# Kernel optimization log

Measured on AMD Instinct MI355X. Metric: run time of the kernel, lower is better.

Reference implementation:

```python
import jax, jax.numpy as jnp
import numpy as np

EPS = 0.25  # diffusion-map epsilon

def setup_inputs() -> dict:
    key = jax.random.key(0)
    ks = jax.random.split(key, 6)
    B, N, F, L = 8, 2048, 256, 16
    s = lambda fan_in: 1.0 / np.sqrt(fan_in)
    return {
        "x":      jax.random.normal(ks[0], (B, N, F), dtype=jnp.float32),
        "proj_w": jax.random.normal(ks[1], (L, F), dtype=jnp.float32) * s(F),
        "proj_b": jnp.zeros((L,), dtype=jnp.float32),
        "pi_w1":  jax.random.normal(ks[2], (F, L), dtype=jnp.float32) * s(L),
        "pi_b1":  jnp.zeros((F,), dtype=jnp.float32),
        "pi_w2":  jax.random.normal(ks[3], (1, F), dtype=jnp.float32) * s(F),
        "pi_b2":  jnp.zeros((1,), dtype=jnp.float32),
        "dt":     jnp.array([0.1], dtype=jnp.float32),
    }

def reference(x, proj_w, proj_b, pi_w1, pi_b1, pi_w2, pi_b2, dt):
    # z = proj(x): [B, N, L]
    z = jnp.einsum("bnf,lf->bnl", x, proj_w) + proj_b
    # pairwise squared distances via expansion (avoids [B,N,N,L] intermediate)
    sq = jnp.sum(z * z, axis=-1)                              # [B, N]
    gram = jnp.einsum("bnl,bml->bnm", z, z)                   # [B, N, N]
    d2 = jnp.maximum(sq[:, :, None] + sq[:, None, :] - 2.0 * gram, 0.0)
    K = jnp.exp(-d2 / (4.0 * EPS))                            # K_epsilon [B,N,N]
    q = jnp.sum(K, axis=2)                                    # q_epsilon_tilde [B,N]
    # pi(z): MLP 16 -> 256 -> 1 with ReLU then Sigmoid
    h = jax.nn.relu(jnp.einsum("bnl,fl->bnf", z, pi_w1) + pi_b1)
    pi_v = jax.nn.sigmoid(jnp.einsum("bnf,of->bno", h, pi_w2) + pi_b2)[..., 0]  # [B,N]
    # K_tilde = K @ diag(pi/q): scale columns
    Kt = K * (pi_v / q)[:, None, :]                            # [B,N,N]
    row = jnp.sum(Kt, axis=2) + 1e-5                           # diag of D_tilde
    # L = (1/eps) * D_tilde^{-1} K_tilde - I ; inverse of diagonal = reciprocal
    # L @ x computed without materializing identity:
    Lx = (1.0 / EPS) * jnp.einsum("bnm,bmf->bnf", Kt / row[:, :, None], x) - x
    return x + dt[0] * Lx
```

## Files before the change

### kernel.cpp

```cpp
#include <hip/hip_runtime.h>
#include <hip/hip_bf16.h>

#define BATCH 8
#define NN    2048
#define FF    256
#define LL    16

typedef float f32x4 __attribute__((ext_vector_type(4)));
typedef short s16x8 __attribute__((ext_vector_type(8)));

static __device__ __forceinline__ unsigned short f2bf(float f) {
    return __builtin_bit_cast(unsigned short, __float2bfloat16(f));
}
static __device__ __forceinline__ float bf2f(unsigned short u) {
    unsigned int x = ((unsigned int)u) << 16;
    return __builtin_bit_cast(float, x);
}

typedef const __attribute__((address_space(1))) unsigned int glb_uint;
typedef __attribute__((address_space(3))) unsigned int lds_uint;
static __device__ __forceinline__ void gload_lds16(const void* g, void* l) {
    __builtin_amdgcn_global_load_lds((glb_uint*)g, (lds_uint*)l, 16, 0, 0);
}

__global__ __launch_bounds__(256) void fused_a_kernel(
    const float* __restrict__ x,
    const float* __restrict__ proj_w, const float* __restrict__ proj_b,
    const float* __restrict__ pi_w1,  const float* __restrict__ pi_b1,
    const float* __restrict__ pi_w2,  const float* __restrict__ pi_b2,
    unsigned short* __restrict__ xT,
    unsigned short* __restrict__ zbG,
    float* __restrict__ sqbuf,
    float* __restrict__ pibuf)
{
    const int bid = blockIdx.x;
    const int b = bid & 7, nt = bid >> 3;
    const int n0 = nt * 32;
    const int t = threadIdx.x;
    const int wv = t >> 6, ln = t & 63;
    const int kg = ln >> 4, cl = ln & 15;

    const float* xb = x + (size_t)b * NN * FF;
    unsigned short* xTb = xT + (size_t)b * FF * NN;

    __shared__ unsigned short xbsh[32 * 268];
    __shared__ unsigned short Wbsh[16 * 268];
    __shared__ unsigned short W1bsh[256 * 24];
    __shared__ unsigned short zbsh[32 * 24];
    __shared__ float b1sh[256], w2sh[256], pbsh[16];
    __shared__ float pp[2][32];

#pragma unroll
    for (int i = 0; i < 8; ++i) {
        const int slot = i * 256 + t;
        const int r = slot >> 6, c4 = slot & 63;
        const float4 v = *(const float4*)(xb + (size_t)(n0 + r) * FF + c4 * 4);
        ushort4 o; o.x = f2bf(v.x); o.y = f2bf(v.y); o.z = f2bf(v.z); o.w = f2bf(v.w);
        *(ushort4*)&xbsh[r * 268 + c4 * 4] = o;
    }
#pragma unroll
    for (int i = 0; i < 4; ++i) {
        const int slot = i * 256 + t;
        const int l = slot >> 6, c4 = slot & 63;
        const float4 v = *(const float4*)(proj_w + l * FF + c4 * 4);
        ushort4 o; o.x = f2bf(v.x); o.y = f2bf(v.y); o.z = f2bf(v.z); o.w = f2bf(v.w);
        *(ushort4*)&Wbsh[l * 268 + c4 * 4] = o;
    }
#pragma unroll
    for (int i = 0; i < 4; ++i) {
        const int slot = i * 256 + t;
        const int f = slot >> 2, q = slot & 3;
        const float4 v = *(const float4*)(pi_w1 + f * LL + q * 4);
        ushort4 o; o.x = f2bf(v.x); o.y = f2bf(v.y); o.z = f2bf(v.z); o.w = f2bf(v.w);
        *(ushort4*)&W1bsh[f * 24 + q * 4] = o;
    }
    b1sh[t] = pi_b1[t];
    w2sh[t] = pi_w2[t];
    if (t < 16) pbsh[t] = proj_b[t];
    __syncthreads();

    if (wv < 2) {
        f32x4 zacc = {0.f, 0.f, 0.f, 0.f};
#pragma unroll
        for (int g = 0; g < 8; ++g) {
            const s16x8 af = *(const s16x8*)&xbsh[(wv * 16 + cl) * 268 + g * 32 + kg * 8];
            const s16x8 bf = *(const s16x8*)&Wbsh[cl * 268 + g * 32 + kg * 8];
            zacc = __builtin_amdgcn_mfma_f32_16x16x32_bf16(af, bf, zacc, 0, 0, 0);
        }
        const float pb = pbsh[cl];
#pragma unroll
        for (int r = 0; r < 4; ++r)
            zbsh[(wv * 16 + kg * 4 + r) * 24 + cl] = f2bf(zacc[r] + pb);
    } else {
#pragma unroll
        for (int it = 0; it < 16; ++it) {
            const int f = (wv - 2) * 128 + it * 8 + (ln >> 3);
            const int q = ln & 7;
            ushort4 o;
            o.x = xbsh[(q * 4 + 0) * 268 + f];
            o.y = xbsh[(q * 4 + 1) * 268 + f];
            o.z = xbsh[(q * 4 + 2) * 268 + f];
            o.w = xbsh[(q * 4 + 3) * 268 + f];
            *(ushort4*)(xTb + (size_t)f * NN + n0 + q * 4) = o;
        }
    }
    __syncthreads();

    if (t < 32) {
        unsigned short zr[16]; float sq = 0.f;
#pragma unroll
        for (int l = 0; l < 16; ++l) {
            zr[l] = zbsh[t * 24 + l];
            const float zf = bf2f(zr[l]);
            sq = fmaf(zf, zf, sq);
        }
        unsigned short* dst = zbG + ((size_t)b * NN + n0 + t) * 16;
        *(uint4*)dst = *(uint4*)&zr[0];
        *(uint4*)(dst + 8) = *(uint4*)&zr[8];
        sqbuf[(size_t)b * NN + n0 + t] = sq;
    }

    {
        const int ntl = wv & 1;
        s16x8 bz = {0, 0, 0, 0, 0, 0, 0, 0};
        if (kg < 2) bz = *(const s16x8*)&zbsh[(ntl * 16 + cl) * 24 + kg * 8];
        float pisum = 0.f;
        const f32x4 zf4 = {0.f, 0.f, 0.f, 0.f};
#pragma unroll
        for (int j = 0; j < 8; ++j) {
            const int ft = (wv >> 1) * 8 + j;
            s16x8 aw = {0, 0, 0, 0, 0, 0, 0, 0};
            if (kg < 2) aw = *(const s16x8*)&W1bsh[(ft * 16 + cl) * 24 + kg * 8];
            const f32x4 h4 = __builtin_amdgcn_mfma_f32_16x16x32_bf16(aw, bz, zf4, 0, 0, 0);
#pragma unroll
            for (int r = 0; r < 4; ++r) {
                const int f = ft * 16 + kg * 4 + r;
                const float h = fmaxf(h4[r] + b1sh[f], 0.f);
                pisum = fmaf(h, w2sh[f], pisum);
            }
        }
        pisum += __shfl_xor(pisum, 16, 64);
        pisum += __shfl_xor(pisum, 32, 64);
        if (ln < 16) pp[wv >> 1][ntl * 16 + ln] = pisum;
    }
    __syncthreads();

    if (t < 32) {
        const float tp = pp[0][t] + pp[1][t] + pi_b2[0];
        pibuf[(size_t)b * NN + n0 + t] = 1.f / (1.f + __expf(-tp));
    }
}

__global__ __launch_bounds__(256) void qc_kernel(
    const unsigned short* __restrict__ zbG,
    const float* __restrict__ sqbuf,
    const float* __restrict__ pibuf,
    float* __restrict__ cbuf)
{
    const int bid = blockIdx.x;
    const int b = bid & 7, nt = bid >> 3;
    const int n0 = nt * 32;
    const int t = threadIdx.x;
    const int wv = t >> 6, ln = t & 63;
    const int kg = ln >> 4, cl = ln & 15;

    const unsigned short* zb = zbG + (size_t)b * NN * LL;
    const float* sqb = sqbuf + (size_t)b * NN;

    __shared__ unsigned short zsh[2][256 * 24];
    __shared__ float sqh[2][256];
    __shared__ float qq[2][32];

    s16x8 zn = {0, 0, 0, 0, 0, 0, 0, 0};
    if (kg < 2) zn = *(const s16x8*)(zb + (size_t)(n0 + (wv & 1) * 16 + cl) * 16 + kg * 8);
    const float sqn = sqb[n0 + (wv & 1) * 16 + cl];
    const f32x4 zf4 = {0.f, 0.f, 0.f, 0.f};
    float qloc = 0.f;

    uint4 za = *(const uint4*)(zb + (size_t)t * 16);
    uint4 zc = *(const uint4*)(zb + (size_t)t * 16 + 8);
    float sv = sqb[t];
    *(uint4*)&zsh[0][t * 24] = za;
    *(uint4*)&zsh[0][t * 24 + 8] = zc;
    sqh[0][t] = sv;
    __syncthreads();

    const int mbase = (wv >> 1) * 128;
    for (int ch = 0; ch < 8; ++ch) {
        const int cur = ch & 1;
        if (ch < 7) {
            const int m = (ch + 1) * 256 + t;
            za = *(const uint4*)(zb + (size_t)m * 16);
            zc = *(const uint4*)(zb + (size_t)m * 16 + 8);
            sv = sqb[m];
        }
#pragma unroll
        for (int mt = 0; mt < 8; ++mt) {
            s16x8 zm = {0, 0, 0, 0, 0, 0, 0, 0};
            if (kg < 2) zm = *(const s16x8*)&zsh[cur][(mbase + mt * 16 + cl) * 24 + kg * 8];
            const f32x4 g = __builtin_amdgcn_mfma_f32_16x16x32_bf16(zm, zn, zf4, 0, 0, 0);
            const f32x4 sq4 = *(const f32x4*)&sqh[cur][mbase + mt * 16 + kg * 4];
#pragma unroll
            for (int r = 0; r < 4; ++r)
                qloc += __expf(2.f * g[r] - sq4[r] - sqn);
        }
        if (ch < 7) {
            *(uint4*)&zsh[cur ^ 1][t * 24] = za;
            *(uint4*)&zsh[cur ^ 1][t * 24 + 8] = zc;
            sqh[cur ^ 1][t] = sv;
        }
        __syncthreads();
    }
    qloc += __shfl_xor(qloc, 16, 64);
    qloc += __shfl_xor(qloc, 32, 64);
    if (ln < 16) qq[wv >> 1][(wv & 1) * 16 + ln] = qloc;
    __syncthreads();
    if (t < 32) {
        const size_t gi = (size_t)b * NN + n0 + t;
        cbuf[gi] = pibuf[gi] / (qq[0][t] + qq[1][t]);
    }
}

struct ZM { s16x8 z[4]; };

__global__ __launch_bounds__(256) void main_kernel(
    const float* __restrict__ x,
    const unsigned short* __restrict__ xT,
    const unsigned short* __restrict__ zbG,
    const float* __restrict__ sqbuf,
    const float* __restrict__ cbuf,
    const float* __restrict__ dtp,
    float* __restrict__ out)
{
    const int bid = blockIdx.x;
    const int b = bid & 7;
    const int rest = bid >> 3;
    const int fs = rest & 1;
    const int nt = rest >> 1;
    const int n0 = nt * 64, f0 = fs * 128;
    const int t = threadIdx.x;
    const int wv = t >> 6, ln = t & 63;
    const int kg = ln >> 4, cl = ln & 15;

    const float*          xb  = x   + (size_t)b * NN * FF;
    const unsigned short* xTb = xT  + (size_t)b * FF * NN;
    const unsigned short* zb  = zbG + (size_t)b * NN * LL;
    const float*          sqB = sqbuf + (size_t)b * NN;
    const float*          cB  = cbuf  + (size_t)b * NN;
    float*                ob  = out + (size_t)b * NN * FF;

    __shared__ unsigned short xsh[2][128 * 64];
    __shared__ unsigned short wsh[2][64 * 64];
    __shared__ float csh[2][64], sqsh[2][64];
    __shared__ float rsp[64];

    const float dtv = dtp[0];
    const int nloc = wv * 16 + cl;

    s16x8 zn = {0, 0, 0, 0, 0, 0, 0, 0};
    if (kg < 2) zn = *(const s16x8*)(zb + (size_t)(n0 + nloc) * 16 + kg * 8);
    const float sqn = sqB[n0 + nloc];
    const f32x4 zf4 = {0.f, 0.f, 0.f, 0.f};

    f32x4 acc[2][4];
#pragma unroll
    for (int fi = 0; fi < 2; ++fi)
#pragma unroll
        for (int ni = 0; ni < 4; ++ni) acc[fi][ni] = (f32x4){0.f, 0.f, 0.f, 0.f};
    float rloc = 0.f;

    auto loadZM = [&](ZM& Z, int kt) {
        const int m0 = kt * 64;
#pragma unroll
        for (int mt = 0; mt < 4; ++mt) {
            Z.z[mt] = (s16x8){0, 0, 0, 0, 0, 0, 0, 0};
            if (kg < 2)
                Z.z[mt] = *(const s16x8*)(zb + (size_t)(m0 + mt * 16 + cl) * 16 + kg * 8);
        }
    };
    auto STAGE_CS = [&](int buf, int kt) {
        const int m0 = kt * 64;
        if (t < 64)        csh[buf][t]       = cB[m0 + t];
        else if (t < 128)  sqsh[buf][t - 64] = sqB[m0 + t - 64];
    };
    auto ISSUE = [&](int buf, int kt) {
        const int m0 = kt * 64;
        char* dst = (char*)&xsh[buf][0];
#pragma unroll
        for (int i = 0; i < 4; ++i) {
            const int fl = (i * 4 + wv) * 8 + (ln >> 3);
            const int cp = ln & 7;
            const int clog = cp ^ (fl & 7);
            const unsigned short* src = xTb + (size_t)(f0 + fl) * NN + m0 + clog * 8;
            gload_lds16(src, dst + (i * 4 + wv) * 1024);
        }
    };
    auto P1 = [&](const ZM& Z, int cur) {
        char* wb = (char*)&wsh[cur][0];
#pragma unroll
        for (int mt = 0; mt < 4; ++mt) {
            const f32x4 g = __builtin_amdgcn_mfma_f32_16x16x32_bf16(Z.z[mt], zn, zf4, 0, 0, 0);
            const f32x4 sq4 = *(const f32x4*)&sqsh[cur][mt * 16 + kg * 4];
            const f32x4 cm4 = *(const f32x4*)&csh[cur][mt * 16 + kg * 4];
            const float w0 = __expf(2.f * g[0] - sq4[0] - sqn) * cm4[0];
            const float w1 = __expf(2.f * g[1] - sq4[1] - sqn) * cm4[1];
            const float w2 = __expf(2.f * g[2] - sq4[2] - sqn) * cm4[2];
            const float w3 = __expf(2.f * g[3] - sq4[3] - sqn) * cm4[3];
            rloc += (w0 + w1) + (w2 + w3);
            uint2 val;
            val.x = (unsigned)f2bf(w0) | ((unsigned)f2bf(w1) << 16);
            val.y = (unsigned)f2bf(w2) | ((unsigned)f2bf(w3) << 16);
            const int c16 = mt * 2 + (kg >> 1);
            const int phys = c16 ^ (nloc & 7);
            *(uint2*)(wb + nloc * 128 + phys * 16 + (kg & 1) * 8) = val;
        }
    };
    auto P2 = [&](int cur) {
        const char* xbuf = (const char*)&xsh[cur][0];
        const char* wbuf = (const char*)&wsh[cur][0];
#pragma unroll
        for (int ks = 0; ks < 2; ++ks) {
            s16x8 a[2], bw[4];
#pragma unroll
            for (int fi = 0; fi < 2; ++fi) {
                const int fl = wv * 32 + fi * 16 + cl;
                const int slot = (ks * 4 + kg) ^ (fl & 7);
                a[fi] = *(const s16x8*)(xbuf + fl * 128 + slot * 16);
            }
#pragma unroll
            for (int ni = 0; ni < 4; ++ni) {
                const int nr = ni * 16 + cl;
                const int slot = (ks * 4 + kg) ^ (nr & 7);
                bw[ni] = *(const s16x8*)(wbuf + nr * 128 + slot * 16);
            }
#pragma unroll
            for (int fi = 0; fi < 2; ++fi)
#pragma unroll
                for (int ni = 0; ni < 4; ++ni)
                    acc[fi][ni] = __builtin_amdgcn_mfma_f32_16x16x32_bf16(
                        a[fi], bw[ni], acc[fi][ni], 0, 0, 0);
        }
    };

    ZM zA, zB;
    STAGE_CS(0, 0);
    loadZM(zA, 0);
    ISSUE(0, 0);
    __syncthreads();

    for (int kt = 0; kt < 32; kt += 2) {
        P1(zA, 0);
        { loadZM(zB, kt + 1); STAGE_CS(1, kt + 1); }
        __syncthreads();
        ISSUE(1, kt + 1);
        __builtin_amdgcn_s_setprio(1);
        P2(0);
        __builtin_amdgcn_s_setprio(0);
        P1(zB, 1);
        if (kt + 2 < 32) { loadZM(zA, kt + 2); STAGE_CS(0, kt + 2); }
        __syncthreads();
        if (kt + 2 < 32) ISSUE(0, kt + 2);
        __builtin_amdgcn_s_setprio(1);
        P2(1);
        __builtin_amdgcn_s_setprio(0);
    }

    rloc += __shfl_xor(rloc, 16, 64);
    rloc += __shfl_xor(rloc, 32, 64);
    if (ln < 16) rsp[wv * 16 + ln] = rloc;
    __syncthreads();

#pragma unroll
    for (int ni = 0; ni < 4; ++ni) {
        const int nl = ni * 16 + cl;
        const float sc = 4.f * dtv / (rsp[nl] + 1e-5f);
        const int ng = n0 + nl;
#pragma unroll
        for (int fi = 0; fi < 2; ++fi) {
            const int fg = f0 + wv * 32 + fi * 16 + kg * 4;
            const float4 xv = *(const float4*)(xb + (size_t)ng * FF + fg);
            float4 o;
            o.x = (1.f - dtv) * xv.x + sc * acc[fi][ni][0];
            o.y = (1.f - dtv) * xv.y + sc * acc[fi][ni][1];
            o.z = (1.f - dtv) * xv.z + sc * acc[fi][ni][2];
            o.w = (1.f - dtv) * xv.w + sc * acc[fi][ni][3];
            *(float4*)(ob + (size_t)ng * FF + fg) = o;
        }
    }
}

extern "C" void kernel_launch(void* const* d_in, const int* in_sizes, int n_in,
                              void* d_out, int out_size, void* d_ws, size_t ws_size,
                              hipStream_t stream) {
    const float* x      = (const float*)d_in[0];
    const float* proj_w = (const float*)d_in[1];
    const float* proj_b = (const float*)d_in[2];
    const float* pi_w1  = (const float*)d_in[3];
    const float* pi_b1  = (const float*)d_in[4];
    const float* pi_w2  = (const float*)d_in[5];
    const float* pi_b2  = (const float*)d_in[6];
    const float* dtp    = (const float*)d_in[7];
    float* out = (float*)d_out;

    unsigned short* xT  = (unsigned short*)d_ws;
    unsigned short* zbG = xT + (size_t)BATCH * FF * NN;
    float* sqbuf = (float*)(zbG + (size_t)BATCH * NN * LL);
    float* pibuf = sqbuf + (size_t)BATCH * NN;
    float* cbuf  = pibuf + (size_t)BATCH * NN;

    fused_a_kernel<<<dim3(BATCH * (NN / 32)), dim3(256), 0, stream>>>(
        x, proj_w, proj_b, pi_w1, pi_b1, pi_w2, pi_b2, xT, zbG, sqbuf, pibuf);

    qc_kernel<<<dim3(BATCH * (NN / 32)), dim3(256), 0, stream>>>(
        zbG, sqbuf, pibuf, cbuf);

    main_kernel<<<dim3(BATCH * (NN / 64) * 2), dim3(256), 0, stream>>>(
        x, xT, zbG, sqbuf, cbuf, dtp, out);
}
```

Before: 148.3 us.

## Fuse three kernels into one persistent kernel with grid barriers and 32x32 MFMA

```diff
diff --git a/kernel.cpp b/kernel.cpp
--- a/kernel.cpp
+++ b/kernel.cpp
@@ -5,9 +5,12 @@
 #define NN    2048
 #define FF    256
 #define LL    16
-
-typedef float f32x4 __attribute__((ext_vector_type(4)));
-typedef short s16x8 __attribute__((ext_vector_type(8)));
+#define GRID  512
+
+typedef float f32x4  __attribute__((ext_vector_type(4)));
+typedef float f32x16 __attribute__((ext_vector_type(16)));
+typedef short s16x8  __attribute__((ext_vector_type(8)));
+typedef unsigned int u32;
 
 static __device__ __forceinline__ unsigned short f2bf(float f) {
     return __builtin_bit_cast(unsigned short, __float2bfloat16(f));
@@ -23,368 +26,344 @@
     __builtin_amdgcn_global_load_lds((glb_uint*)g, (lds_uint*)l, 16, 0, 0);
 }
 
-__global__ __launch_bounds__(256) void fused_a_kernel(
+union Smem {
+    struct {
+        unsigned short xbsh[32 * 268];
+        unsigned short Wbsh[16 * 268];
+        unsigned short W1bsh[256 * 24];
+        unsigned short zbsh[32 * 24];
+        float b1sh[256], w2sh[256], pbsh[16];
+        float pp[2][32];
+    } a;
+    struct {
+        unsigned short zsh[2][256 * 24];
+        float sqh[2][256];
+        float qq[2][32];
+    } q;
+    struct {
+        unsigned short xsh[2][8192];
+        float rsp[4][32];
+    } m;
+};
+
+static __device__ __forceinline__ void gsync(unsigned* cnt) {
+    __syncthreads();
+    if (threadIdx.x == 0) {
+        __threadfence();
+        __hip_atomic_fetch_add(cnt, 1u, __ATOMIC_ACQ_REL, __HIP_MEMORY_SCOPE_AGENT);
+        while (__hip_atomic_load(cnt, __ATOMIC_ACQUIRE, __HIP_MEMORY_SCOPE_AGENT) < GRID) {
+            __builtin_amdgcn_s_sleep(2);
+        }
+    }
+    __syncthreads();
+    __threadfence();
+}
+
+__global__ __launch_bounds__(256, 2) void tmd_fused(
     const float* __restrict__ x,
     const float* __restrict__ proj_w, const float* __restrict__ proj_b,
     const float* __restrict__ pi_w1,  const float* __restrict__ pi_b1,
     const float* __restrict__ pi_w2,  const float* __restrict__ pi_b2,
+    const float* __restrict__ dtp,
     unsigned short* __restrict__ xT,
     unsigned short* __restrict__ zbG,
     float* __restrict__ sqbuf,
-    float* __restrict__ pibuf)
+    float* __restrict__ pibuf,
+    float* __restrict__ cebuf,
+    unsigned* __restrict__ syncA,
+    unsigned* __restrict__ syncQ,
+    float* __restrict__ out)
 {
+    __shared__ Smem sm;
     const int bid = blockIdx.x;
-    const int b = bid & 7, nt = bid >> 3;
-    const int n0 = nt * 32;
+    const int b = bid & 7;
     const int t = threadIdx.x;
     const int wv = t >> 6, ln = t & 63;
     const int kg = ln >> 4, cl = ln & 15;
 
     const float* xb = x + (size_t)b * NN * FF;
     unsigned short* xTb = xT + (size_t)b * FF * NN;
-
-    __shared__ unsigned short xbsh[32 * 268];
-    __shared__ unsigned short Wbsh[16 * 268];
-    __shared__ unsigned short W1bsh[256 * 24];
-    __shared__ unsigned short zbsh[32 * 24];
-    __shared__ float b1sh[256], w2sh[256], pbsh[16];
-    __shared__ float pp[2][32];
-
-#pragma unroll
-    for (int i = 0; i < 8; ++i) {
-        const int slot = i * 256 + t;
-        const int r = slot >> 6, c4 = slot & 63;
-        const float4 v = *(const float4*)(xb + (size_t)(n0 + r) * FF + c4 * 4);
-        ushort4 o; o.x = f2bf(v.x); o.y = f2bf(v.y); o.z = f2bf(v.z); o.w = f2bf(v.w);
-        *(ushort4*)&xbsh[r * 268 + c4 * 4] = o;
+    unsigned short* zbW = zbG + (size_t)b * NN * LL;
+    const unsigned short* zb = zbG + (size_t)b * NN * LL;
+    float* sqW = sqbuf + (size_t)b * NN;
+    const float* sqB = sqbuf + (size_t)b * NN;
+
+    {
+        const int nt = bid >> 3;
+        const int n0 = nt * 32;
+        auto& A = sm.a;
+
+#pragma unroll
+        for (int i = 0; i < 8; ++i) {
+            const int slot = i * 256 + t;
+            const int r = slot >> 6, c4 = slot & 63;
+            const float4 v = *(const float4*)(xb + (size_t)(n0 + r) * FF + c4 * 4);
+            ushort4 o; o.x = f2bf(v.x); o.y = f2bf(v.y); o.z = f2bf(v.z); o.w = f2bf(v.w);
+            *(ushort4*)&A.xbsh[r * 268 + c4 * 4] = o;
+        }
+#pragma unroll
+        for (int i = 0; i < 4; ++i) {
+            const int slot = i * 256 + t;
+            const int l = slot >> 6, c4 = slot & 63;
+            const float4 v = *(const float4*)(proj_w + l * FF + c4 * 4);
+            ushort4 o; o.x = f2bf(v.x); o.y = f2bf(v.y); o.z = f2bf(v.z); o.w = f2bf(v.w);
+            *(ushort4*)&A.Wbsh[l * 268 + c4 * 4] = o;
+        }
+#pragma unroll
+        for (int i = 0; i < 4; ++i) {
+            const int slot = i * 256 + t;
+            const int f = slot >> 2, q = slot & 3;
+            const float4 v = *(const float4*)(pi_w1 + f * LL + q * 4);
+            ushort4 o; o.x = f2bf(v.x); o.y = f2bf(v.y); o.z = f2bf(v.z); o.w = f2bf(v.w);
+            *(ushort4*)&A.W1bsh[f * 24 + q * 4] = o;
+        }
+        A.b1sh[t] = pi_b1[t];
+        A.w2sh[t] = pi_w2[t];
+        if (t < 16) A.pbsh[t] = proj_b[t];
+        __syncthreads();
+
+        if (wv < 2) {
+            f32x4 zacc = {0.f, 0.f, 0.f, 0.f};
+#pragma unroll
+            for (int g = 0; g < 8; ++g) {
+                const s16x8 af = *(const s16x8*)&A.xbsh[(wv * 16 + cl) * 268 + g * 32 + kg * 8];
+                const s16x8 bf = *(const s16x8*)&A.Wbsh[cl * 268 + g * 32 + kg * 8];
+                zacc = __builtin_amdgcn_mfma_f32_16x16x32_bf16(af, bf, zacc, 0, 0, 0);
+            }
+            const float pb = A.pbsh[cl];
+#pragma unroll
+            for (int r = 0; r < 4; ++r)
+                A.zbsh[(wv * 16 + kg * 4 + r) * 24 + cl] = f2bf(zacc[r] + pb);
+        } else {
+#pragma unroll
+            for (int it = 0; it < 16; ++it) {
+                const int f = (wv - 2) * 128 + it * 8 + (ln >> 3);
+                const int q = ln & 7;
+                ushort4 o;
+                o.x = A.xbsh[(q * 4 + 0) * 268 + f];
+                o.y = A.xbsh[(q * 4 + 1) * 268 + f];
+                o.z = A.xbsh[(q * 4 + 2) * 268 + f];
+                o.w = A.xbsh[(q * 4 + 3) * 268 + f];
+                *(ushort4*)(xTb + (size_t)f * NN + n0 + q * 4) = o;
+            }
+        }
+        __syncthreads();
+
+        if (t < 32) {
+            unsigned short zr[16]; float sq = 0.f;
+#pragma unroll
+            for (int l = 0; l < 16; ++l) {
+                zr[l] = A.zbsh[t * 24 + l];
+                const float zf = bf2f(zr[l]);
+                sq = fmaf(zf, zf, sq);
+            }
+            unsigned short* dst = zbW + (size_t)(n0 + t) * 16;
+            *(uint4*)dst = *(uint4*)&zr[0];
+            *(uint4*)(dst + 8) = *(uint4*)&zr[8];
+            sqW[n0 + t] = sq;
+        }
+
+        {
+            const int ntl = wv & 1;
+            s16x8 bz = {0, 0, 0, 0, 0, 0, 0, 0};
+            if (kg < 2) bz = *(const s16x8*)&A.zbsh[(ntl * 16 + cl) * 24 + kg * 8];
+            float pisum = 0.f;
+            const f32x4 zf4 = {0.f, 0.f, 0.f, 0.f};
+#pragma unroll
+            for (int j = 0; j < 8; ++j) {
+                const int ft = (wv >> 1) * 8 + j;
+                s16x8 aw = {0, 0, 0, 0, 0, 0, 0, 0};
+                if (kg < 2) aw = *(const s16x8*)&A.W1bsh[(ft * 16 + cl) * 24 + kg * 8];
+                const f32x4 h4 = __builtin_amdgcn_mfma_f32_16x16x32_bf16(aw, bz, zf4, 0, 0, 0);
+#pragma unroll
+                for (int r = 0; r < 4; ++r) {
+                    const int f = ft * 16 + kg * 4 + r;
+                    const float hh = fmaxf(h4[r] + A.b1sh[f], 0.f);
+                    pisum = fmaf(hh, A.w2sh[f], pisum);
+                }
+            }
+            pisum += __shfl_xor(pisum, 16, 64);
+            pisum += __shfl_xor(pisum, 32, 64);
+            if (ln < 16) A.pp[wv >> 1][ntl * 16 + ln] = pisum;
+        }
+        __syncthreads();
+        if (t < 32) {
+            const float tp = A.pp[0][t] + A.pp[1][t] + pi_b2[0];
+            pibuf[(size_t)b * NN + n0 + t] = 1.f / (1.f + __expf(-tp));
+        }
     }
-#pragma unroll
-    for (int i = 0; i < 4; ++i) {
-        const int slot = i * 256 + t;
-        const int l = slot >> 6, c4 = slot & 63;
-        const float4 v = *(const float4*)(proj_w + l * FF + c4 * 4);
-        ushort4 o; o.x = f2bf(v.x); o.y = f2bf(v.y); o.z = f2bf(v.z); o.w = f2bf(v.w);
-        *(ushort4*)&Wbsh[l * 268 + c4 * 4] = o;
+
+    gsync(syncA);
+
+    {
+        const int nt = bid >> 3;
+        const int n0 = nt * 32;
+        auto& Q = sm.q;
+
+        s16x8 zn = {0, 0, 0, 0, 0, 0, 0, 0};
+        if (kg < 2) zn = *(const s16x8*)(zb + (size_t)(n0 + (wv & 1) * 16 + cl) * 16 + kg * 8);
+        const float sqn = sqB[n0 + (wv & 1) * 16 + cl];
+        const f32x4 zf4 = {0.f, 0.f, 0.f, 0.f};
+        float qloc = 0.f;
+
+        uint4 za = *(const uint4*)(zb + (size_t)t * 16);
+        uint4 zc = *(const uint4*)(zb + (size_t)t * 16 + 8);
+        float sv = sqB[t];
+        *(uint4*)&Q.zsh[0][t * 24] = za;
+        *(uint4*)&Q.zsh[0][t * 24 + 8] = zc;
+        Q.sqh[0][t] = sv;
+        __syncthreads();
+
+        const int mbase = (wv >> 1) * 128;
+        for (int ch = 0; ch < 8; ++ch) {
+            const int cur = ch & 1;
+            if (ch < 7) {
+                const int m = (ch + 1) * 256 + t;
+                za = *(const uint4*)(zb + (size_t)m * 16);
+                zc = *(const uint4*)(zb + (size_t)m * 16 + 8);
+                sv = sqB[m];
+            }
+#pragma unroll
+            for (int mt = 0; mt < 8; ++mt) {
+                s16x8 zm = {0, 0, 0, 0, 0, 0, 0, 0};
+                if (kg < 2) zm = *(const s16x8*)&Q.zsh[cur][(mbase + mt * 16 + cl) * 24 + kg * 8];
+                const f32x4 g = __builtin_amdgcn_mfma_f32_16x16x32_bf16(zm, zn, zf4, 0, 0, 0);
+                const f32x4 sq4 = *(const f32x4*)&Q.sqh[cur][mbase + mt * 16 + kg * 4];
+#pragma unroll
+                for (int r = 0; r < 4; ++r)
+                    qloc += __expf(2.f * g[r] - sq4[r] - sqn);
+            }
+            if (ch < 7) {
+                *(uint4*)&Q.zsh[cur ^ 1][t * 24] = za;
+                *(uint4*)&Q.zsh[cur ^ 1][t * 24 + 8] = zc;
+                Q.sqh[cur ^ 1][t] = sv;
+            }
+            __syncthreads();
+        }
+        qloc += __shfl_xor(qloc, 16, 64);
+        qloc += __shfl_xor(qloc, 32, 64);
+        if (ln < 16) Q.qq[wv >> 1][(wv & 1) * 16 + ln] = qloc;
+        __syncthreads();
+        if (t < 32) {
+            const size_t gi = (size_t)b * NN + n0 + t;
+            cebuf[gi] = pibuf[gi] / (Q.qq[0][t] + Q.qq[1][t]) * __expf(-sqB[n0 + t]);
+        }
     }
-#pragma unroll
-    for (int i = 0; i < 4; ++i) {
-        const int slot = i * 256 + t;
-        const int f = slot >> 2, q = slot & 3;
-        const float4 v = *(const float4*)(pi_w1 + f * LL + q * 4);
-        ushort4 o; o.x = f2bf(v.x); o.y = f2bf(v.y); o.z = f2bf(v.z); o.w = f2bf(v.w);
-        *(ushort4*)&W1bsh[f * 24 + q * 4] = o;
-    }
-    b1sh[t] = pi_b1[t];
-    w2sh[t] = pi_w2[t];
-    if (t < 16) pbsh[t] = proj_b[t];
-    __syncthreads();
-
-    if (wv < 2) {
-        f32x4 zacc = {0.f, 0.f, 0.f, 0.f};
-#pragma unroll
-        for (int g = 0; g < 8; ++g) {
-            const s16x8 af = *(const s16x8*)&xbsh[(wv * 16 + cl) * 268 + g * 32 + kg * 8];
-            const s16x8 bf = *(const s16x8*)&Wbsh[cl * 268 + g * 32 + kg * 8];
-            zacc = __builtin_amdgcn_mfma_f32_16x16x32_bf16(af, bf, zacc, 0, 0, 0);
-        }
-        const float pb = pbsh[cl];
-#pragma unroll
-        for (int r = 0; r < 4; ++r)
-            zbsh[(wv * 16 + kg * 4 + r) * 24 + cl] = f2bf(zacc[r] + pb);
-    } else {
-#pragma unroll
-        for (int it = 0; it < 16; ++it) {
-            const int f = (wv - 2) * 128 + it * 8 + (ln >> 3);
-            const int q = ln & 7;
-            ushort4 o;
-            o.x = xbsh[(q * 4 + 0) * 268 + f];
-            o.y = xbsh[(q * 4 + 1) * 268 + f];
-            o.z = xbsh[(q * 4 + 2) * 268 + f];
-            o.w = xbsh[(q * 4 + 3) * 268 + f];
-            *(ushort4*)(xTb + (size_t)f * NN + n0 + q * 4) = o;
-        }
-    }
-    __syncthreads();
-
-    if (t < 32) {
-        unsigned short zr[16]; float sq = 0.f;
-#pragma unroll
-        for (int l = 0; l < 16; ++l) {
-            zr[l] = zbsh[t * 24 + l];
-            const float zf = bf2f(zr[l]);
-            sq = fmaf(zf, zf, sq);
-        }
-        unsigned short* dst = zbG + ((size_t)b * NN + n0 + t) * 16;
-        *(uint4*)dst = *(uint4*)&zr[0];
-        *(uint4*)(dst + 8) = *(uint4*)&zr[8];
-        sqbuf[(size_t)b * NN + n0 + t] = sq;
-    }
+
+    gsync(syncQ);
 
     {
-        const int ntl = wv & 1;
-        s16x8 bz = {0, 0, 0, 0, 0, 0, 0, 0};
-        if (kg < 2) bz = *(const s16x8*)&zbsh[(ntl * 16 + cl) * 24 + kg * 8];
-        float pisum = 0.f;
-        const f32x4 zf4 = {0.f, 0.f, 0.f, 0.f};
-#pragma unroll
-        for (int j = 0; j < 8; ++j) {
-            const int ft = (wv >> 1) * 8 + j;
-            s16x8 aw = {0, 0, 0, 0, 0, 0, 0, 0};
-            if (kg < 2) aw = *(const s16x8*)&W1bsh[(ft * 16 + cl) * 24 + kg * 8];
-            const f32x4 h4 = __builtin_amdgcn_mfma_f32_16x16x32_bf16(aw, bz, zf4, 0, 0, 0);
-#pragma unroll
-            for (int r = 0; r < 4; ++r) {
-                const int f = ft * 16 + kg * 4 + r;
-                const float h = fmaxf(h4[r] + b1sh[f], 0.f);
-                pisum = fmaf(h, w2sh[f], pisum);
-            }
-        }
-        pisum += __shfl_xor(pisum, 16, 64);
-        pisum += __shfl_xor(pisum, 32, 64);
-        if (ln < 16) pp[wv >> 1][ntl * 16 + ln] = pisum;
-    }
-    __syncthreads();
-
-    if (t < 32) {
-        const float tp = pp[0][t] + pp[1][t] + pi_b2[0];
-        pibuf[(size_t)b * NN + n0 + t] = 1.f / (1.f + __expf(-tp));
-    }
-}
-
-__global__ __launch_bounds__(256) void qc_kernel(
-    const unsigned short* __restrict__ zbG,
-    const float* __restrict__ sqbuf,
-    const float* __restrict__ pibuf,
-    float* __restrict__ cbuf)
-{
-    const int bid = blockIdx.x;
-    const int b = bid & 7, nt = bid >> 3;
-    const int n0 = nt * 32;
-    const int t = threadIdx.x;
-    const int wv = t >> 6, ln = t & 63;
-    const int kg = ln >> 4, cl = ln & 15;
-
-    const unsigned short* zb = zbG + (size_t)b * NN * LL;
-    const float* sqb = sqbuf + (size_t)b * NN;
-
-    __shared__ unsigned short zsh[2][256 * 24];
-    __shared__ float sqh[2][256];
-    __shared__ float qq[2][32];
-
-    s16x8 zn = {0, 0, 0, 0, 0, 0, 0, 0};
-    if (kg < 2) zn = *(const s16x8*)(zb + (size_t)(n0 + (wv & 1) * 16 + cl) * 16 + kg * 8);
-    const float sqn = sqb[n0 + (wv & 1) * 16 + cl];
-    const f32x4 zf4 = {0.f, 0.f, 0.f, 0.f};
-    float qloc = 0.f;
-
-    uint4 za = *(const uint4*)(zb + (size_t)t * 16);
-    uint4 zc = *(const uint4*)(zb + (size_t)t * 16 + 8);
-    float sv = sqb[t];
-    *(uint4*)&zsh[0][t * 24] = za;
-    *(uint4*)&zsh[0][t * 24 + 8] = zc;
-    sqh[0][t] = sv;
-    __syncthreads();
-
-    const int mbase = (wv >> 1) * 128;
-    for (int ch = 0; ch < 8; ++ch) {
-        const int cur = ch & 1;
-        if (ch < 7) {
-            const int m = (ch + 1) * 256 + t;
-            za = *(const uint4*)(zb + (size_t)m * 16);
-            zc = *(const uint4*)(zb + (size_t)m * 16 + 8);
-            sv = sqb[m];
-        }
-#pragma unroll
-        for (int mt = 0; mt < 8; ++mt) {
-            s16x8 zm = {0, 0, 0, 0, 0, 0, 0, 0};
-            if (kg < 2) zm = *(const s16x8*)&zsh[cur][(mbase + mt * 16 + cl) * 24 + kg * 8];
-            const f32x4 g = __builtin_amdgcn_mfma_f32_16x16x32_bf16(zm, zn, zf4, 0, 0, 0);
-            const f32x4 sq4 = *(const f32x4*)&sqh[cur][mbase + mt * 16 + kg * 4];
-#pragma unroll
-            for (int r = 0; r < 4; ++r)
-                qloc += __expf(2.f * g[r] - sq4[r] - sqn);
-        }
-        if (ch < 7) {
-            *(uint4*)&zsh[cur ^ 1][t * 24] = za;
-            *(uint4*)&zsh[cur ^ 1][t * 24 + 8] = zc;
-            sqh[cur ^ 1][t] = sv;
-        }
-        __syncthreads();
-    }
-    qloc += __shfl_xor(qloc, 16, 64);
-    qloc += __shfl_xor(qloc, 32, 64);
-    if (ln < 16) qq[wv >> 1][(wv & 1) * 16 + ln] = qloc;
-    __syncthreads();
-    if (t < 32) {
-        const size_t gi = (size_t)b * NN + n0 + t;
-        cbuf[gi] = pibuf[gi] / (qq[0][t] + qq[1][t]);
-    }
-}
-
-struct ZM { s16x8 z[4]; };
-
-__global__ __launch_bounds__(256) void main_kernel(
-    const float* __restrict__ x,
-    const unsigned short* __restrict__ xT,
-    const unsigned short* __restrict__ zbG,
-    const float* __restrict__ sqbuf,
-    const float* __restrict__ cbuf,
-    const float* __restrict__ dtp,
-    float* __restrict__ out)
-{
-    const int bid = blockIdx.x;
-    const int b = bid & 7;
-    const int rest = bid >> 3;
-    const int fs = rest & 1;
-    const int nt = rest >> 1;
-    const int n0 = nt * 64, f0 = fs * 128;
-    const int t = threadIdx.x;
-    const int wv = t >> 6, ln = t & 63;
-    const int kg = ln >> 4, cl = ln & 15;
-
-    const float*          xb  = x   + (size_t)b * NN * FF;
-    const unsigned short* xTb = xT  + (size_t)b * FF * NN;
-    const unsigned short* zb  = zbG + (size_t)b * NN * LL;
-    const float*          sqB = sqbuf + (size_t)b * NN;
-    const float*          cB  = cbuf  + (size_t)b * NN;
-    float*                ob  = out + (size_t)b * NN * FF;
-
-    __shared__ unsigned short xsh[2][128 * 64];
-    __shared__ unsigned short wsh[2][64 * 64];
-    __shared__ float csh[2][64], sqsh[2][64];
-    __shared__ float rsp[64];
-
-    const float dtv = dtp[0];
-    const int nloc = wv * 16 + cl;
-
-    s16x8 zn = {0, 0, 0, 0, 0, 0, 0, 0};
-    if (kg < 2) zn = *(const s16x8*)(zb + (size_t)(n0 + nloc) * 16 + kg * 8);
-    const float sqn = sqB[n0 + nloc];
-    const f32x4 zf4 = {0.f, 0.f, 0.f, 0.f};
-
-    f32x4 acc[2][4];
-#pragma unroll
-    for (int fi = 0; fi < 2; ++fi)
-#pragma unroll
-        for (int ni = 0; ni < 4; ++ni) acc[fi][ni] = (f32x4){0.f, 0.f, 0.f, 0.f};
-    float rloc = 0.f;
-
-    auto loadZM = [&](ZM& Z, int kt) {
-        const int m0 = kt * 64;
-#pragma unroll
-        for (int mt = 0; mt < 4; ++mt) {
-            Z.z[mt] = (s16x8){0, 0, 0, 0, 0, 0, 0, 0};
-            if (kg < 2)
-                Z.z[mt] = *(const s16x8*)(zb + (size_t)(m0 + mt * 16 + cl) * 16 + kg * 8);
-        }
-    };
-    auto STAGE_CS = [&](int buf, int kt) {
-        const int m0 = kt * 64;
-        if (t < 64)        csh[buf][t]       = cB[m0 + t];
-        else if (t < 128)  sqsh[buf][t - 64] = sqB[m0 + t - 64];
-    };
-    auto ISSUE = [&](int buf, int kt) {
-        const int m0 = kt * 64;
-        char* dst = (char*)&xsh[buf][0];
-#pragma unroll
-        for (int i = 0; i < 4; ++i) {
-            const int fl = (i * 4 + wv) * 8 + (ln >> 3);
-            const int cp = ln & 7;
-            const int clog = cp ^ (fl & 7);
-            const unsigned short* src = xTb + (size_t)(f0 + fl) * NN + m0 + clog * 8;
-            gload_lds16(src, dst + (i * 4 + wv) * 1024);
-        }
-    };
-    auto P1 = [&](const ZM& Z, int cur) {
-        char* wb = (char*)&wsh[cur][0];
-#pragma unroll
-        for (int mt = 0; mt < 4; ++mt) {
-            const f32x4 g = __builtin_amdgcn_mfma_f32_16x16x32_bf16(Z.z[mt], zn, zf4, 0, 0, 0);
-            const f32x4 sq4 = *(const f32x4*)&sqsh[cur][mt * 16 + kg * 4];
-            const f32x4 cm4 = *(const f32x4*)&csh[cur][mt * 16 + kg * 4];
-            const float w0 = __expf(2.f * g[0] - sq4[0] - sqn) * cm4[0];
-            const float w1 = __expf(2.f * g[1] - sq4[1] - sqn) * cm4[1];
-            const float w2 = __expf(2.f * g[2] - sq4[2] - sqn) * cm4[2];
-            const float w3 = __expf(2.f * g[3] - sq4[3] - sqn) * cm4[3];
-            rloc += (w0 + w1) + (w2 + w3);
-            uint2 val;
-            val.x = (unsigned)f2bf(w0) | ((unsigned)f2bf(w1) << 16);
-            val.y = (unsigned)f2bf(w2) | ((unsigned)f2bf(w3) << 16);
-            const int c16 = mt * 2 + (kg >> 1);
-            const int phys = c16 ^ (nloc & 7);
-            *(uint2*)(wb + nloc * 128 + phys * 16 + (kg & 1) * 8) = val;
-        }
-    };
-    auto P2 = [&](int cur) {
-        const char* xbuf = (const char*)&xsh[cur][0];
-        const char* wbuf = (const char*)&wsh[cur][0];
-#pragma unroll
-        for (int ks = 0; ks < 2; ++ks) {
-            s16x8 a[2], bw[4];
-#pragma unroll
-            for (int fi = 0; fi < 2; ++fi) {
-                const int fl = wv * 32 + fi * 16 + cl;
-                const int slot = (ks * 4 + kg) ^ (fl & 7);
-                a[fi] = *(const s16x8*)(xbuf + fl * 128 + slot * 16);
-            }
-#pragma unroll
-            for (int ni = 0; ni < 4; ++ni) {
-                const int nr = ni * 16 + cl;
-                const int slot = (ks * 4 + kg) ^ (nr & 7);
-                bw[ni] = *(const s16x8*)(wbuf + nr * 128 + slot * 16);
-            }
-#pragma unroll
-            for (int fi = 0; fi < 2; ++fi)
-#pragma unroll
-                for (int ni = 0; ni < 4; ++ni)
-                    acc[fi][ni] = __builtin_amdgcn_mfma_f32_16x16x32_bf16(
-                        a[fi], bw[ni], acc[fi][ni], 0, 0, 0);
-        }
-    };
-
-    ZM zA, zB;
-    STAGE_CS(0, 0);
-    loadZM(zA, 0);
-    ISSUE(0, 0);
-    __syncthreads();
-
-    for (int kt = 0; kt < 32; kt += 2) {
-        P1(zA, 0);
-        { loadZM(zB, kt + 1); STAGE_CS(1, kt + 1); }
-        __syncthreads();
-        ISSUE(1, kt + 1);
-        __builtin_amdgcn_s_setprio(1);
-        P2(0);
-        __builtin_amdgcn_s_setprio(0);
-        P1(zB, 1);
-        if (kt + 2 < 32) { loadZM(zA, kt + 2); STAGE_CS(0, kt + 2); }
-        __syncthreads();
-        if (kt + 2 < 32) ISSUE(0, kt + 2);
-        __builtin_amdgcn_s_setprio(1);
-        P2(1);
-        __builtin_amdgcn_s_setprio(0);
-    }
-
-    rloc += __shfl_xor(rloc, 16, 64);
-    rloc += __shfl_xor(rloc, 32, 64);
-    if (ln < 16) rsp[wv * 16 + ln] = rloc;
-    __syncthreads();
-
-#pragma unroll
-    for (int ni = 0; ni < 4; ++ni) {
-        const int nl = ni * 16 + cl;
-        const float sc = 4.f * dtv / (rsp[nl] + 1e-5f);
-        const int ng = n0 + nl;
-#pragma unroll
-        for (int fi = 0; fi < 2; ++fi) {
-            const int fg = f0 + wv * 32 + fi * 16 + kg * 4;
-            const float4 xv = *(const float4*)(xb + (size_t)ng * FF + fg);
-            float4 o;
-            o.x = (1.f - dtv) * xv.x + sc * acc[fi][ni][0];
-            o.y = (1.f - dtv) * xv.y + sc * acc[fi][ni][1];
-            o.z = (1.f - dtv) * xv.z + sc * acc[fi][ni][2];
-            o.w = (1.f - dtv) * xv.w + sc * acc[fi][ni][3];
-            *(float4*)(ob + (size_t)ng * FF + fg) = o;
+        const int fs = (bid >> 3) & 1;
+        const int nt = bid >> 4;
+        const int n0 = nt * 64, f0 = fs * 128;
+        const int i31 = ln & 31, h = ln >> 5;
+        const int nt_w = wv & 1, fs_w = wv >> 1;
+
+        const float* ceB = cebuf + (size_t)b * NN;
+        float* ob = out + (size_t)b * NN * FF;
+        const float dtv = dtp[0];
+
+        const f32x16 Z16 = {0.f,0.f,0.f,0.f,0.f,0.f,0.f,0.f,
+                            0.f,0.f,0.f,0.f,0.f,0.f,0.f,0.f};
+
+        const s16x8 zn = *(const s16x8*)(zb + (size_t)(n0 + nt_w * 32 + i31) * 16 + h * 8);
+        const float sqn = sqB[n0 + nt_w * 32 + i31];
+
+        f32x16 acc0 = Z16, acc1 = Z16;
+        float rloc = 0.f;
+
+        auto ISSUE = [&](char* dstBase, int kt) {
+            const int m0 = kt * 64;
+#pragma unroll
+            for (int i = 0; i < 4; ++i) {
+                const int fl = (i * 4 + wv) * 8 + (ln >> 3);
+                const int cp = ln & 7;
+                const int clog = cp ^ (fl & 7);
+                gload_lds16(xTb + (size_t)(f0 + fl) * NN + m0 + clog * 8,
+                            dstBase + (i * 4 + wv) * 1024);
+            }
+        };
+        auto LOADZM = [&](int mG) -> s16x8 {
+            return *(const s16x8*)(zb + (size_t)(mG + i31) * 16 + h * 8);
+        };
+
+        auto COMPUTE = [&](int kt, const char* xbuf,
+                           const s16x8 zc0, const s16x8 zc1,
+                           s16x8& zn0, s16x8& zn1, int ktN) {
+            s16x8 Afr[2][2];
+#pragma unroll
+            for (int g = 0; g < 2; ++g) {
+                const s16x8 zm = g ? zc1 : zc0;
+                const int mG = kt * 64 + g * 32;
+                const f32x16 gD = __builtin_amdgcn_mfma_f32_32x32x16_bf16(zm, zn, Z16, 0, 0, 0);
+                u32 pk[8];
+#pragma unroll
+                for (int q = 0; q < 4; ++q) {
+                    const f32x4 ce4 = *(const f32x4*)(ceB + mG + 4 * h + 8 * q);
+                    const float w0 = __expf(2.f * gD[q * 4 + 0] - sqn) * ce4[0];
+                    const float w1 = __expf(2.f * gD[q * 4 + 1] - sqn) * ce4[1];
+                    const float w2 = __expf(2.f * gD[q * 4 + 2] - sqn) * ce4[2];
+                    const float w3 = __expf(2.f * gD[q * 4 + 3] - sqn) * ce4[3];
+                    rloc += (w0 + w1) + (w2 + w3);
+                    pk[q * 2 + 0] = (u32)f2bf(w0) | ((u32)f2bf(w1) << 16);
+                    pk[q * 2 + 1] = (u32)f2bf(w2) | ((u32)f2bf(w3) << 16);
+                }
+                u32 sw[8];
+#pragma unroll
+                for (int p = 0; p < 8; ++p) sw[p] = (u32)__shfl_xor((int)pk[p], 32, 64);
+                union { u32 u[4]; s16x8 v; } a0, a1;
+                a0.u[0] = h ? sw[2] : pk[0];  a0.u[1] = h ? sw[3] : pk[1];
+                a0.u[2] = h ? pk[2] : sw[0];  a0.u[3] = h ? pk[3] : sw[1];
+                a1.u[0] = h ? sw[6] : pk[4];  a1.u[1] = h ? sw[7] : pk[5];
+                a1.u[2] = h ? pk[6] : sw[4];  a1.u[3] = h ? pk[7] : sw[5];
+                Afr[g][0] = a0.v;  Afr[g][1] = a1.v;
+            }
+            zn0 = LOADZM(ktN * 64);
+            zn1 = LOADZM(ktN * 64 + 32);
+            const int fl0 = fs_w * 64 + i31;
+            const int fl1 = fl0 + 32;
+#pragma unroll
+            for (int g = 0; g < 2; ++g)
+#pragma unroll
+                for (int mk = 0; mk < 2; ++mk) {
+                    const int c = g * 4 + mk * 2 + h;
+                    const s16x8 B0 = *(const s16x8*)(xbuf + fl0 * 128 + (c ^ (fl0 & 7)) * 16);
+                    acc0 = __builtin_amdgcn_mfma_f32_32x32x16_bf16(Afr[g][mk], B0, acc0, 0, 0, 0);
+                    const s16x8 B1 = *(const s16x8*)(xbuf + fl1 * 128 + (c ^ (fl1 & 7)) * 16);
+                    acc1 = __builtin_amdgcn_mfma_f32_32x32x16_bf16(Afr[g][mk], B1, acc1, 0, 0, 0);
+                }
+        };
+
+        ISSUE((char*)sm.m.xsh[0], 0);
+        s16x8 zmA0 = LOADZM(0), zmA1 = LOADZM(32);
+        s16x8 zmB0, zmB1;
+
+        for (int kt = 0; kt < 32; kt += 2) {
+            __syncthreads();
+            ISSUE((char*)sm.m.xsh[1], kt + 1);
+            COMPUTE(kt, (const char*)sm.m.xsh[0], zmA0, zmA1, zmB0, zmB1, kt + 1);
+            __syncthreads();
+            if (kt + 2 < 32) ISSUE((char*)sm.m.xsh[0], kt + 2);
+            COMPUTE(kt + 1, (const char*)sm.m.xsh[1], zmB0, zmB1, zmA0, zmA1,
+                    (kt + 2 < 32) ? kt + 2 : 0);
+        }
+
+        rloc += __shfl_xor(rloc, 32, 64);
+        if (h == 0) sm.m.rsp[wv][i31] = rloc;
+
+#pragma unroll
+        for (int ft = 0; ft < 2; ++ft) {
+            const f32x16 accv = ft ? acc1 : acc0;
+            const int fg = f0 + fs_w * 64 + ft * 32 + i31;
+#pragma unroll
+            for (int r = 0; r < 16; ++r) {
+                const int nl = (r & 3) + 8 * (r >> 2) + 4 * h;
+                const float rstot = sm.m.rsp[wv][nl] + 1e-5f;
+                const float sc = 4.f * dtv / rstot;
+                const int ng = n0 + nt_w * 32 + nl;
+                const float xv = xb[(size_t)ng * FF + fg];
+                ob[(size_t)ng * FF + fg] = (1.f - dtv) * xv + sc * accv[r];
+            }
         }
     }
 }
@@ -406,14 +385,12 @@
     unsigned short* zbG = xT + (size_t)BATCH * FF * NN;
     float* sqbuf = (float*)(zbG + (size_t)BATCH * NN * LL);
     float* pibuf = sqbuf + (size_t)BATCH * NN;
-    float* cbuf  = pibuf + (size_t)BATCH * NN;
-
-    fused_a_kernel<<<dim3(BATCH * (NN / 32)), dim3(256), 0, stream>>>(
-        x, proj_w, proj_b, pi_w1, pi_b1, pi_w2, pi_b2, xT, zbG, sqbuf, pibuf);
-
-    qc_kernel<<<dim3(BATCH * (NN / 32)), dim3(256), 0, stream>>>(
-        zbG, sqbuf, pibuf, cbuf);
-
-    main_kernel<<<dim3(BATCH * (NN / 64) * 2), dim3(256), 0, stream>>>(
-        x, xT, zbG, sqbuf, cbuf, dtp, out);
-}
+    float* cebuf = pibuf + (size_t)BATCH * NN;
+    unsigned* syncp = (unsigned*)(cebuf + (size_t)BATCH * NN);
+
+    hipMemsetAsync(syncp, 0, 2 * sizeof(unsigned), stream);
+
+    tmd_fused<<<dim3(GRID), dim3(256), 0, stream>>>(
+        x, proj_w, proj_b, pi_w1, pi_b1, pi_w2, pi_b2, dtp,
+        xT, zbG, sqbuf, pibuf, cebuf, syncp, syncp + 1, out);
+}
```

New measurement: 279.8 us. 1.89x slower.
